# Optimization experiments

Measured on AMD Instinct MI355X. Metric: run time of the kernel, lower is better.

Reference implementation:

```python
import jax, jax.numpy as jnp
import numpy as np

N_NODES = 100000
N_EDGES = 300000
HIDDEN = 256

def _lin_init(key, fan_in, fan_out):
    return jax.random.normal(key, (fan_in, fan_out), jnp.float32) / np.sqrt(fan_in)

def setup_inputs():
    key = jax.random.key(0)
    ks = jax.random.split(key, 16)
    x = jax.random.randint(ks[0], (N_NODES, 16), 0, 11).astype(jnp.float32)
    edge_index = jax.random.randint(ks[1], (2, N_EDGES), 0, N_NODES)
    edge_attr = jax.random.randint(ks[2], (N_EDGES, 4), 0, 5).astype(jnp.float32)
    batch = jnp.sort(jax.random.randint(ks[3], (N_NODES,), 0, 256))
    atom_emb = jax.random.normal(ks[4], (11, 64), jnp.float32)
    bond_emb_table = jax.random.normal(ks[5], (5, 64), jnp.float32)
    vp_w1 = _lin_init(ks[6], 64, 32); vp_b1 = jnp.zeros((32,), jnp.float32)
    vp_w2 = _lin_init(ks[7], 32, 8)
    # chemical-knowledge bias init: max_valence - 1 for atom types 0..7 (bias dim is 8)
    vp_b2 = jnp.array([3., 2., 1., 5., 0., 0., 0., 0.], jnp.float32)
    gnn_wself = jax.random.normal(ks[8], (3, HIDDEN, HIDDEN), jnp.float32) / np.sqrt(HIDDEN)
    gnn_bself = jnp.zeros((3, HIDDEN), jnp.float32)
    gnn_wmsg = jax.random.normal(ks[9], (3, HIDDEN + 64, HIDDEN), jnp.float32) / np.sqrt(HIDDEN + 64)
    gnn_bmsg = jnp.zeros((3, HIDDEN), jnp.float32)
    bc_w1 = _lin_init(ks[10], 2 * HIDDEN + 2, 128); bc_b1 = jnp.zeros((128,), jnp.float32)
    bc_w2 = _lin_init(ks[11], 128, 64); bc_b2 = jnp.zeros((64,), jnp.float32)
    bc_w3 = _lin_init(ks[12], 64, 4); bc_b3 = jnp.zeros((4,), jnp.float32)
    cp_w1 = _lin_init(ks[13], HIDDEN, 128); cp_b1 = jnp.zeros((128,), jnp.float32)
    cp_w2 = _lin_init(ks[14], 128, 32); cp_b2 = jnp.zeros((32,), jnp.float32)
    return dict(x=x, edge_attr=edge_attr, atom_emb=atom_emb, bond_emb_table=bond_emb_table,
                vp_w1=vp_w1, vp_b1=vp_b1, vp_w2=vp_w2, vp_b2=vp_b2,
                gnn_wself=gnn_wself, gnn_bself=gnn_bself, gnn_wmsg=gnn_wmsg, gnn_bmsg=gnn_bmsg,
                bc_w1=bc_w1, bc_b1=bc_b1, bc_w2=bc_w2, bc_b2=bc_b2, bc_w3=bc_w3, bc_b3=bc_b3,
                cp_w1=cp_w1, cp_b1=cp_b1, cp_w2=cp_w2, cp_b2=cp_b2,
                edge_index=edge_index, batch=batch)

def _forward(x, edge_attr, atom_emb, bond_emb_table, vp_w1, vp_b1, vp_w2, vp_b2,
             gnn_wself, gnn_bself, gnn_wmsg, gnn_bmsg,
             bc_w1, bc_b1, bc_w2, bc_b2, bc_w3, bc_b3,
             cp_w1, cp_b1, cp_w2, cp_b2, edge_index, batch):
    relu = jax.nn.relu
    n = x.shape[0]
    atom_types = jnp.clip(x[:, 0].astype(jnp.int32), 0, 10)        # [N]
    ae = atom_emb[atom_types]                                      # [N, 64]
    valence_logits = relu(ae @ vp_w1 + vp_b1) @ vp_w2 + vp_b2      # [N, 8]
    pv = jnp.argmax(valence_logits, axis=-1) + 1                   # [N] predicted valences in [1,8]
    bt = jnp.clip(edge_attr[:, 0].astype(jnp.int32), 0, 4)
    be = bond_emb_table[bt]                                        # [E, 64]
    h = jnp.concatenate([ae, jax.nn.one_hot(pv - 1, 8, dtype=ae.dtype)], axis=-1)  # [N, 72]
    h = jnp.pad(h, ((0, 0), (0, HIDDEN - h.shape[1])))             # pad to [N, HIDDEN]
    row, col = edge_index[0], edge_index[1]
    # stacked ChemicalConstraintGNN layers (message passing with bond-type features)
    for l in range(3):
        msg = relu(jnp.concatenate([h[col], be], axis=-1) @ gnn_wmsg[l] + gnn_bmsg[l])  # [E, H]
        agg = jax.ops.segment_sum(msg, row, num_segments=n)
        h = relu(h @ gnn_wself[l] + gnn_bself[l] + agg)
    # ValenceConstraintLayer: damp nodes whose degree exceeds predicted valence
    degree = jax.ops.segment_sum(jnp.ones(row.shape[0], h.dtype), row, num_segments=n)
    violations = relu(degree - pv.astype(h.dtype))                 # [N]
    h = h / (1.0 + violations)[:, None]
    # constrained bond prediction
    bf = jnp.concatenate([h[row], h[col],
                          pv[row][:, None].astype(h.dtype), pv[col][:, None].astype(h.dtype)], axis=-1)
    bl = relu(relu(bf @ bc_w1 + bc_b1) @ bc_w2 + bc_b2) @ bc_w3 + bc_b3  # [E, 4]
    # vectorized chemical constraints (replaces per-edge Python loop)
    at_r, at_c = atom_types[row], atom_types[col]
    halogen = ((at_r == 4) | (at_r == 5) | (at_c == 4) | (at_c == 5)).astype(bl.dtype)
    lowval2 = ((pv[row] <= 2) | (pv[col] <= 2)).astype(bl.dtype)
    lowval1 = ((pv[row] <= 1) | (pv[col] <= 1)).astype(bl.dtype)
    penalty = jnp.zeros_like(bl)
    penalty = penalty.at[:, 1:].add((-100.0 * halogen - 50.0 * lowval1)[:, None])
    penalty = penalty.at[:, 2].add(-50.0 * lowval2)
    bond_logits = bl + penalty
    chem_props = relu(h @ cp_w1 + cp_b1) @ cp_w2 + cp_b2           # [N, 32]
    return h, chem_props, valence_logits, bond_logits, violations

def reference(x, edge_attr, atom_emb, bond_emb_table, vp_w1, vp_b1, vp_w2, vp_b2,
              gnn_wself, gnn_bself, gnn_wmsg, gnn_bmsg,
              bc_w1, bc_b1, bc_w2, bc_b2, bc_w3, bc_b3,
              cp_w1, cp_b1, cp_w2, cp_b2, edge_index, batch):
    return _forward(x, edge_attr, atom_emb, bond_emb_table, vp_w1, vp_b1, vp_w2, vp_b2,
                    gnn_wself, gnn_bself, gnn_wmsg, gnn_bmsg,
                    bc_w1, bc_b1, bc_w2, bc_b2, bc_w3, bc_b3,
                    cp_w1, cp_b1, cp_w2, cp_b2, edge_index, batch)
```

## Files before the change

### kernel.cpp

```cpp
#include <hip/hip_runtime.h>

#define N_NODES 100000
#define N_EDGES 300000
#define M_PAD   100096
#define E_PAD   300032

typedef unsigned short u16;
typedef short bf16x8 __attribute__((ext_vector_type(8)));
typedef float f32x4  __attribute__((ext_vector_type(4)));
typedef unsigned short u16x8 __attribute__((ext_vector_type(8)));

__device__ __forceinline__ float bf2f(u16 u) {
    unsigned x = ((unsigned)u) << 16;
    return __builtin_bit_cast(float, x);
}
__device__ __forceinline__ u16 f2bf(float f) {
    unsigned u = __builtin_bit_cast(unsigned, f);
    unsigned r = (u + 0x7FFF + ((u >> 16) & 1)) >> 16;
    return (u16)r;
}

#define H_OFF   0
#define CP_OFF  25600000
#define VL_OFF  28800000
#define BL_OFF  29600000
#define VI_OFF  30800000

#define GLL(gp, lp) __builtin_amdgcn_global_load_lds( \
    (const __attribute__((address_space(1))) unsigned int*)(gp), \
    (__attribute__((address_space(3))) unsigned int*)(lp), 16, 0, 0)

__global__ void k_type_mlp(const float* __restrict__ atom_emb,
                           const float* __restrict__ vp_w1, const float* __restrict__ vp_b1,
                           const float* __restrict__ vp_w2, const float* __restrict__ vp_b2,
                           int* __restrict__ pv_tab, float* __restrict__ vl_tab,
                           float* __restrict__ h0_tab)
{
    int tid = threadIdx.x;
    for (int i = tid; i < 11 * 256; i += 256) h0_tab[i] = 0.f;
    __syncthreads();
    if (tid < 11) {
        int t = tid;
        const float* ae = atom_emb + t * 64;
        float lg[8];
        #pragma unroll
        for (int c = 0; c < 8; ++c) lg[c] = vp_b2[c];
        for (int j = 0; j < 32; ++j) {
            float z = vp_b1[j];
            for (int d = 0; d < 64; ++d) z += ae[d] * vp_w1[d * 32 + j];
            z = fmaxf(z, 0.f);
            #pragma unroll
            for (int c = 0; c < 8; ++c) lg[c] += z * vp_w2[j * 8 + c];
        }
        int best = 0;
        #pragma unroll
        for (int c = 1; c < 8; ++c) if (lg[c] > lg[best]) best = c;
        pv_tab[t] = best + 1;
        for (int c = 0; c < 8; ++c) vl_tab[t * 8 + c] = lg[c];
        float* h0 = h0_tab + t * 256;
        for (int d = 0; d < 64; ++d) h0[d] = ae[d];
        h0[64 + best] = 1.f;
    }
}

__global__ void k_tables(const float* __restrict__ bond_emb,
                         const float* __restrict__ gnn_wself, const float* __restrict__ gnn_bself,
                         const float* __restrict__ gnn_wmsg, const float* __restrict__ gnn_bmsg,
                         const float* __restrict__ h0_tab,
                         float* __restrict__ self0_tab, float* __restrict__ msg0_tab,
                         float* __restrict__ bondtab)
{
    int b = blockIdx.x, c = threadIdx.x;
    if (b < 11) {
        int t = b;
        const float* h0 = h0_tab + t * 256;
        float acc = gnn_bself[c];
        for (int k = 0; k < 256; ++k) acc += h0[k] * gnn_wself[k * 256 + c];
        self0_tab[t * 256 + c] = acc;
    } else if (b < 66) {
        int idx = b - 11; int t = idx / 5, bb = idx % 5;
        const float* h0 = h0_tab + t * 256;
        float acc = gnn_bmsg[c];
        for (int k = 0; k < 256; ++k) acc += h0[k] * gnn_wmsg[k * 256 + c];
        const float* be = bond_emb + bb * 64;
        for (int k = 0; k < 64; ++k) acc += be[k] * gnn_wmsg[(256 + k) * 256 + c];
        msg0_tab[idx * 256 + c] = fmaxf(acc, 0.f);
    } else {
        int idx = b - 66; int l = idx / 5 + 1, bb = idx % 5;
        const float* w = gnn_wmsg + (size_t)l * 320 * 256;
        const float* be = bond_emb + bb * 64;
        float acc = gnn_bmsg[l * 256 + c];
        for (int k = 0; k < 64; ++k) acc += be[k] * w[(256 + k) * 256 + c];
        bondtab[(l - 1) * 5 * 256 + bb * 256 + c] = acc;
    }
}

__global__ void k_wtrans(const float* __restrict__ wmsg, const float* __restrict__ wself,
                         const float* __restrict__ bcw1, const float* __restrict__ cpw1,
                         const float* __restrict__ bcw2, const float* __restrict__ cpw2,
                         u16* __restrict__ BtL1, u16* __restrict__ BtL2, u16* __restrict__ Bt3,
                         u16* __restrict__ BtW2, u16* __restrict__ BtCP2)
{
    int b = blockIdx.x, k = threadIdx.x;
    if (b < 512) {
        int n = b;
        float v = (n < 256) ? wmsg[(size_t)1 * 320 * 256 + (size_t)k * 256 + n]
                            : wself[(size_t)1 * 256 * 256 + (size_t)k * 256 + (n - 256)];
        BtL1[n * 256 + k] = f2bf(v);
    } else if (b < 1024) {
        int n = b - 512;
        float v = (n < 256) ? wmsg[(size_t)2 * 320 * 256 + (size_t)k * 256 + n]
                            : wself[(size_t)2 * 256 * 256 + (size_t)k * 256 + (n - 256)];
        BtL2[n * 256 + k] = f2bf(v);
    } else if (b < 1408) {
        int n = b - 1024;
        float v;
        if (n < 128)      v = bcw1[k * 128 + n];
        else if (n < 256) v = bcw1[(256 + k) * 128 + (n - 128)];
        else              v = cpw1[k * 128 + (n - 256)];
        Bt3[n * 256 + k] = f2bf(v);
    } else if (b < 1536) {
        int n = b - 1408;
        if (k < 128) BtW2[n * 128 + k] = f2bf(n < 64 ? bcw2[k * 64 + n] : 0.f);
    } else {
        int n = b - 1536;
        if (k < 128) BtCP2[n * 128 + k] = f2bf(n < 32 ? cpw2[k * 32 + n] : 0.f);
    }
}

__global__ void k_setup_bias(const float* __restrict__ bself, const float* __restrict__ bcb1,
                             const float* __restrict__ cpb1,
                             float* __restrict__ bias512, float* __restrict__ biasPost)
{
    int i = blockIdx.x * 256 + threadIdx.x;
    if (i < 1024) {
        int l = i >> 9, c = i & 511;
        bias512[l * 512 + c] = (c < 256) ? 0.f : bself[(l + 1) * 256 + (c - 256)];
    } else if (i < 1408) {
        int c = i - 1024;
        biasPost[c] = (c < 128) ? bcb1[c] : ((c < 256) ? 0.f : cpb1[c - 256]);
    }
}

__global__ void k_node_init(const float* __restrict__ x, const int* __restrict__ pv_tab,
                            const float* __restrict__ vl_tab,
                            int* __restrict__ types, int* __restrict__ pvarr,
                            int* __restrict__ degree, float* __restrict__ vl_out)
{
    int i = blockIdx.x * blockDim.x + threadIdx.x;
    if (i >= N_NODES) return;
    int t = (int)x[i * 16];
    t = min(max(t, 0), 10);
    types[i] = t;
    pvarr[i] = pv_tab[t];
    degree[i] = 0;
    float4 v0 = *(const float4*)&vl_tab[t * 8];
    float4 v1 = *(const float4*)&vl_tab[t * 8 + 4];
    *(float4*)&vl_out[i * 8]     = v0;
    *(float4*)&vl_out[i * 8 + 4] = v1;
}

__global__ void k_edge_deg(const int* __restrict__ ei, int* __restrict__ degree)
{
    int e = blockIdx.x * blockDim.x + threadIdx.x;
    if (e >= N_EDGES) return;
    atomicAdd(&degree[ei[e]], 1);
}

#define SCAN_B 1024
__global__ void k_scan1(const int* __restrict__ degree, int* __restrict__ part, int* __restrict__ bsum)
{
    __shared__ int s[SCAN_B];
    int tid = threadIdx.x;
    int i = blockIdx.x * SCAN_B + tid;
    int v = (i < N_NODES) ? degree[i] : 0;
    s[tid] = v; __syncthreads();
    for (int off = 1; off < SCAN_B; off <<= 1) {
        int t = (tid >= off) ? s[tid - off] : 0;
        __syncthreads();
        s[tid] += t;
        __syncthreads();
    }
    if (i < N_NODES) part[i] = s[tid] - v;
    if (tid == SCAN_B - 1) bsum[blockIdx.x] = s[tid];
}

__global__ void k_scan2(const int* __restrict__ bsum, int* __restrict__ bbase, int nb)
{
    __shared__ int s[128];
    int tid = threadIdx.x;
    int v = (tid < nb) ? bsum[tid] : 0;
    s[tid] = v; __syncthreads();
    for (int off = 1; off < 128; off <<= 1) {
        int t = (tid >= off) ? s[tid - off] : 0;
        __syncthreads();
        s[tid] += t;
        __syncthreads();
    }
    bbase[tid] = s[tid] - v;
}

__global__ void k_scan3(int* __restrict__ part, const int* __restrict__ bbase, int* __restrict__ cursor)
{
    int i = blockIdx.x * SCAN_B + threadIdx.x;
    if (i >= N_NODES) return;
    int o = part[i] + bbase[blockIdx.x];
    part[i] = o;
    cursor[i] = o;
}

__global__ void k_csr_fill(const int* __restrict__ ei, const float* __restrict__ edge_attr,
                           const int* __restrict__ types, int* __restrict__ cursor,
                           int* __restrict__ csr, int* __restrict__ rowcsr, int* __restrict__ eidarr)
{
    int e = blockIdx.x * blockDim.x + threadIdx.x;
    if (e >= N_EDGES) return;
    int row = ei[e], col = ei[N_EDGES + e];
    int bt = (int)edge_attr[e * 4];
    bt = min(max(bt, 0), 4);
    int pos = atomicAdd(&cursor[row], 1);
    csr[pos] = col | (bt << 20) | (types[col] << 24);
    rowcsr[pos] = row;
    eidarr[pos] = e;
}

__global__ __launch_bounds__(256) void k_agg0(const int* __restrict__ offsets, const int* __restrict__ degree,
                       const int* __restrict__ types,
                       const float* __restrict__ self0_tab, const float* __restrict__ msg0_tab,
                       const int* __restrict__ csr, u16* __restrict__ h)
{
    int wid = threadIdx.x >> 6, lane = threadIdx.x & 63;
    int node = blockIdx.x * 4 + wid;
    if (node >= N_NODES) return;
    int t = types[node];
    float4 acc = *(const float4*)&self0_tab[t * 256 + lane * 4];
    int start = offsets[node], deg = degree[node];
    for (int j = 0; j < deg; ++j) {
        int p = csr[start + j];
        int combo = ((p >> 24) & 0xF) * 5 + ((p >> 20) & 7);
        float4 m = *(const float4*)&msg0_tab[combo * 256 + lane * 4];
        acc.x += m.x; acc.y += m.y; acc.z += m.z; acc.w += m.w;
    }
    ushort4 r;
    r.x = f2bf(fmaxf(acc.x, 0.f)); r.y = f2bf(fmaxf(acc.y, 0.f));
    r.z = f2bf(fmaxf(acc.z, 0.f)); r.w = f2bf(fmaxf(acc.w, 0.f));
    *(ushort4*)&h[(size_t)node * 256 + lane * 4] = r;
}

__global__ __launch_bounds__(256) void k_agg12(const int* __restrict__ offsets, const int* __restrict__ degree,
                        const u16* __restrict__ hs, const u16* __restrict__ hm,
                        const float* __restrict__ bondtab, const int* __restrict__ csr,
                        u16* __restrict__ h, int final_layer, const int* __restrict__ pvarr,
                        float* __restrict__ h_out, u16* __restrict__ hd_bf, float* __restrict__ viol_out)
{
    int wid = threadIdx.x >> 6, lane = threadIdx.x & 63;
    int node = blockIdx.x * 4 + wid;
    if (node >= N_NODES) return;
    ushort4 s4 = *(const ushort4*)&hs[(size_t)node * 256 + lane * 4];
    float ax = bf2f(s4.x), ay = bf2f(s4.y), az = bf2f(s4.z), aw = bf2f(s4.w);
    int start = offsets[node], deg = degree[node];
    for (int j = 0; j < deg; ++j) {
        int p = csr[start + j];
        int c = p & 0xFFFFF;
        int bt = (p >> 20) & 7;
        ushort4 m4 = *(const ushort4*)&hm[(size_t)c * 256 + lane * 4];
        float4 bb = *(const float4*)&bondtab[bt * 256 + lane * 4];
        ax += fmaxf(bf2f(m4.x) + bb.x, 0.f);
        ay += fmaxf(bf2f(m4.y) + bb.y, 0.f);
        az += fmaxf(bf2f(m4.z) + bb.z, 0.f);
        aw += fmaxf(bf2f(m4.w) + bb.w, 0.f);
    }
    ax = fmaxf(ax, 0.f); ay = fmaxf(ay, 0.f); az = fmaxf(az, 0.f); aw = fmaxf(aw, 0.f);
    if (!final_layer) {
        ushort4 r;
        r.x = f2bf(ax); r.y = f2bf(ay); r.z = f2bf(az); r.w = f2bf(aw);
        *(ushort4*)&h[(size_t)node * 256 + lane * 4] = r;
    } else {
        float viol = fmaxf((float)deg - (float)pvarr[node], 0.f);
        float s = 1.f / (1.f + viol);
        ax *= s; ay *= s; az *= s; aw *= s;
        float4 v = make_float4(ax, ay, az, aw);
        *(float4*)&h_out[(size_t)node * 256 + lane * 4] = v;
        ushort4 r;
        r.x = f2bf(ax); r.y = f2bf(ay); r.z = f2bf(az); r.w = f2bf(aw);
        *(ushort4*)&hd_bf[(size_t)node * 256 + lane * 4] = r;
        if (lane == 0) viol_out[node] = viol;
    }
}

__global__ __launch_bounds__(256) void k_gemm_dual(
    const u16* __restrict__ A, const u16* __restrict__ Bt,
    const float* __restrict__ bias512,
    u16* __restrict__ Dm, u16* __restrict__ Ds, int M, int MT)
{
    __shared__ u16 S[24576];
    u16* As = S;
    u16* Bs = S + 4096;
    u16* Cs = S + 8192;
    int b = blockIdx.x;
    int rsub = b & 31;
    int nt = rsub >> 3, m8 = rsub & 7;
    int mt = (b >> 5) * 8 + m8;
    if (mt >= MT) return;
    int bm = mt * 128, bn = nt * 128;

    int t = threadIdx.x;
    int lane = t & 63, w = t >> 6;
    int wm = w & 1, wn = w >> 1;
    f32x4 zero = {0.f, 0.f, 0.f, 0.f};
    f32x4 acc[4][4];
    #pragma unroll
    for (int i = 0; i < 4; ++i)
        #pragma unroll
        for (int j = 0; j < 4; ++j) acc[i][j] = zero;

    int arow = t >> 2, acol = (t & 3) * 8;
    const u16* Ag = A + (size_t)(bm + arow) * 256 + acol;
    const u16* Bg = Bt + (size_t)(bn + arow) * 256 + acol;
    u16* Asp = As + t * 8;
    u16* Bsp = Bs + t * 8;
    int q = lane >> 4, r = lane & 15;

    for (int k0 = 0; k0 < 256; k0 += 32) {
        __syncthreads();
        GLL(Ag + k0,            Asp);
        GLL(Ag + 64 * 256 + k0, Asp + 2048);
        GLL(Bg + k0,            Bsp);
        GLL(Bg + 64 * 256 + k0, Bsp + 2048);
        __syncthreads();
        bf16x8 af[4], bfr[4];
        #pragma unroll
        for (int i = 0; i < 4; ++i)
            af[i] = *(const bf16x8*)&As[(wm * 64 + i * 16 + r) * 32 + q * 8];
        #pragma unroll
        for (int j = 0; j < 4; ++j)
            bfr[j] = *(const bf16x8*)&Bs[(wn * 64 + j * 16 + r) * 32 + q * 8];
        #pragma unroll
        for (int i = 0; i < 4; ++i)
            #pragma unroll
            for (int j = 0; j < 4; ++j)
                acc[i][j] = __builtin_amdgcn_mfma_f32_16x16x32_bf16(af[i], bfr[j], acc[i][j], 0, 0, 0);
    }
    #pragma unroll
    for (int i = 0; i < 4; ++i) {
        int rowl = wm * 64 + i * 16 + q * 4;
        #pragma unroll
        for (int j = 0; j < 4; ++j) {
            int coll = wn * 64 + j * 16 + r;
            float bv = bias512[bn + coll];
            #pragma unroll
            for (int rr = 0; rr < 4; ++rr)
                Cs[(rowl + rr) * 128 + coll] = f2bf(acc[i][j][rr] + bv);
        }
    }
    __syncthreads();
    u16* Dbase = (nt < 2) ? (Dm + bn) : (Ds + (bn - 256));
    int c16 = (t & 15) * 8, rbase = t >> 4;
    #pragma unroll
    for (int g = 0; g < 8; ++g) {
        int rowl = rbase + g * 16;
        int rowg = bm + rowl;
        if (rowg < M) {
            u16x8 v = *(const u16x8*)&Cs[rowl * 128 + c16];
            *(u16x8*)&Dbase[(size_t)rowg * 256 + c16] = v;
        }
    }
}

__global__ __launch_bounds__(256) void k_gemm_post(
    const u16* __restrict__ A, const u16* __restrict__ Bt3,
    const float* __restrict__ biasPost,
    u16* __restrict__ UV, u16* __restrict__ CP1, int M, int MT)
{
    __shared__ u16 S[24576];
    u16* As = S;
    u16* Bs = S + 4096;
    u16* Cs = S + 8192;
    int b = blockIdx.x;
    int rsub = b % 24;
    int nt = rsub >> 3, m8 = rsub & 7;
    int mt = (b / 24) * 8 + m8;
    if (mt >= MT) return;
    int bm = mt * 128, bn = nt * 128;

    int t = threadIdx.x;
    int lane = t & 63, w = t >> 6;
    int wm = w & 1, wn = w >> 1;
    f32x4 zero = {0.f, 0.f, 0.f, 0.f};
    f32x4 acc[4][4];
    #pragma unroll
    for (int i = 0; i < 4; ++i)
        #pragma unroll
        for (int j = 0; j < 4; ++j) acc[i][j] = zero;

    int arow = t >> 2, acol = (t & 3) * 8;
    const u16* Ag = A + (size_t)(bm + arow) * 256 + acol;
    const u16* Bg = Bt3 + (size_t)(bn + arow) * 256 + acol;
    u16* Asp = As + t * 8;
    u16* Bsp = Bs + t * 8;
    int q = lane >> 4, r = lane & 15;

    for (int k0 = 0; k0 < 256; k0 += 32) {
        __syncthreads();
        GLL(Ag + k0,            Asp);
        GLL(Ag + 64 * 256 + k0, Asp + 2048);
        GLL(Bg + k0,            Bsp);
        GLL(Bg + 64 * 256 + k0, Bsp + 2048);
        __syncthreads();
        bf16x8 af[4], bfr[4];
        #pragma unroll
        for (int i = 0; i < 4; ++i)
            af[i] = *(const bf16x8*)&As[(wm * 64 + i * 16 + r) * 32 + q * 8];
        #pragma unroll
        for (int j = 0; j < 4; ++j)
            bfr[j] = *(const bf16x8*)&Bs[(wn * 64 + j * 16 + r) * 32 + q * 8];
        #pragma unroll
        for (int i = 0; i < 4; ++i)
            #pragma unroll
            for (int j = 0; j < 4; ++j)
                acc[i][j] = __builtin_amdgcn_mfma_f32_16x16x32_bf16(af[i], bfr[j], acc[i][j], 0, 0, 0);
    }
    #pragma unroll
    for (int i = 0; i < 4; ++i) {
        int rowl = wm * 64 + i * 16 + q * 4;
        #pragma unroll
        for (int j = 0; j < 4; ++j) {
            int coll = wn * 64 + j * 16 + r;
            float bv = biasPost[bn + coll];
            #pragma unroll
            for (int rr = 0; rr < 4; ++rr) {
                float val = acc[i][j][rr] + bv;
                if (nt == 2) val = fmaxf(val, 0.f);
                Cs[(rowl + rr) * 128 + coll] = f2bf(val);
            }
        }
    }
    __syncthreads();
    int c16 = (t & 15) * 8, rbase = t >> 4;
    #pragma unroll
    for (int g = 0; g < 8; ++g) {
        int rowl = rbase + g * 16;
        int rowg = bm + rowl;
        if (rowg < M) {
            u16x8 v = *(const u16x8*)&Cs[rowl * 128 + c16];
            if (nt < 2) *(u16x8*)&UV[(size_t)rowg * 256 + bn + c16] = v;
            else        *(u16x8*)&CP1[(size_t)rowg * 128 + c16] = v;
        }
    }
}

__global__ __launch_bounds__(256) void k_gemm_k128(
    const u16* __restrict__ A, const u16* __restrict__ Bt,
    const float* __restrict__ bias, float* __restrict__ C,
    int ldc, int M, int N)
{
    __shared__ u16 As[4096];
    __shared__ u16 Bs[4096];
    int t = threadIdx.x;
    int lane = t & 63, w = t >> 6;
    int wm = w & 1, wn = w >> 1;
    int bm = blockIdx.x * 128;
    int arow = t >> 2, acol = (t & 3) * 8;
    int q = lane >> 4, r = lane & 15;
    const u16* Ag = A + (size_t)(bm + arow) * 128 + acol;
    const u16* Bg = Bt + (size_t)arow * 128 + acol;
    f32x4 zero = {0.f, 0.f, 0.f, 0.f};
    f32x4 acc[4][4];
    #pragma unroll
    for (int i = 0; i < 4; ++i)
        #pragma unroll
        for (int j = 0; j < 4; ++j) acc[i][j] = zero;

    for (int kc = 0; kc < 4; ++kc) {
        __syncthreads();
        GLL(Ag + kc * 32,            As + t * 8);
        GLL(Ag + 64 * 128 + kc * 32, As + 2048 + t * 8);
        GLL(Bg + kc * 32,            Bs + t * 8);
        GLL(Bg + 64 * 128 + kc * 32, Bs + 2048 + t * 8);
        __syncthreads();
        bf16x8 af[4], bfr[4];
        #pragma unroll
        for (int i = 0; i < 4; ++i)
            af[i] = *(const bf16x8*)&As[(wm * 64 + i * 16 + r) * 32 + q * 8];
        #pragma unroll
        for (int j = 0; j < 4; ++j)
            bfr[j] = *(const bf16x8*)&Bs[(wn * 64 + j * 16 + r) * 32 + q * 8];
        #pragma unroll
        for (int i = 0; i < 4; ++i)
            #pragma unroll
            for (int j = 0; j < 4; ++j)
                acc[i][j] = __builtin_amdgcn_mfma_f32_16x16x32_bf16(af[i], bfr[j], acc[i][j], 0, 0, 0);
    }
    #pragma unroll
    for (int i = 0; i < 4; ++i) {
        int rowb = bm + wm * 64 + i * 16 + q * 4;
        #pragma unroll
        for (int j = 0; j < 4; ++j) {
            int colg = wn * 64 + j * 16 + r;
            if (colg >= N) continue;
            float bv = bias[colg];
            #pragma unroll
            for (int rr = 0; rr < 4; ++rr) {
                int rowg = rowb + rr;
                if (rowg < M) C[(size_t)rowg * ldc + colg] = acc[i][j][rr] + bv;
            }
        }
    }
}

__global__ __launch_bounds__(256) void k_bond_fused(
    const int* __restrict__ csr, const int* __restrict__ rowcsr, const int* __restrict__ eidarr,
    const int* __restrict__ types, const int* __restrict__ pvarr, const int* __restrict__ pv_tab,
    const u16* __restrict__ uv, const float* __restrict__ bc_w1,
    const u16* __restrict__ BtW2, const float* __restrict__ bc_b2,
    const float* __restrict__ bc_w3, const float* __restrict__ bc_b3,
    float* __restrict__ bl_out)
{
    __shared__ u16 T1s[16384];
    __shared__ u16 Bs[16384];
    __shared__ float w5s[128], w6s[128], W3s[256], b2s[64], b3s[4];
    __shared__ int pvts[16];

    int t = threadIdx.x;
    int p0 = blockIdx.x * 128;

    if (t < 128) { w5s[t] = bc_w1[512 * 128 + t]; w6s[t] = bc_w1[513 * 128 + t]; }
    if (t < 256) W3s[t] = bc_w3[t];
    if (t < 64) b2s[t] = bc_b2[t];
    if (t < 4)  b3s[t] = bc_b3[t];
    if (t < 11) pvts[t] = pv_tab[t];
    #pragma unroll
    for (int c = 0; c < 4; ++c) {
        GLL(BtW2 + (size_t)(t >> 2) * 128 + c * 32 + (t & 3) * 8,        Bs + c * 4096 + t * 8);
        GLL(BtW2 + (size_t)(64 + (t >> 2)) * 128 + c * 32 + (t & 3) * 8, Bs + c * 4096 + 2048 + t * 8);
    }

    int l = t >> 1;
    int half = t & 1;
    int pos = p0 + l;
    int prow = 0, pk = 0;
    if (pos < N_EDGES) { prow = rowcsr[pos]; pk = csr[pos]; }
    int pcol = pk & 0xFFFFF;
    float pvr = (float)pvarr[prow];
    __syncthreads();
    float pvc = (float)pvts[(pk >> 24) & 0xF];

    const u16* up = uv + (size_t)prow * 256 + half * 64;
    const u16* vp = uv + (size_t)pcol * 256 + 128 + half * 64;
    #pragma unroll
    for (int j = 0; j < 8; ++j) {
        int c = half * 64 + j * 8;
        ushort4 ua = *(const ushort4*)(up + j * 8);
        ushort4 ub = *(const ushort4*)(up + j * 8 + 4);
        ushort4 va = *(const ushort4*)(vp + j * 8);
        ushort4 vb = *(const ushort4*)(vp + j * 8 + 4);
        int chunk = c >> 5, kk = c & 31;
        u16* dst = T1s + chunk * 4096 + l * 32 + kk;
        dst[0] = f2bf(fmaxf(bf2f(ua.x) + bf2f(va.x) + pvr * w5s[c+0] + pvc * w6s[c+0], 0.f));
        dst[1] = f2bf(fmaxf(bf2f(ua.y) + bf2f(va.y) + pvr * w5s[c+1] + pvc * w6s[c+1], 0.f));
        dst[2] = f2bf(fmaxf(bf2f(ua.z) + bf2f(va.z) + pvr * w5s[c+2] + pvc * w6s[c+2], 0.f));
        dst[3] = f2bf(fmaxf(bf2f(ua.w) + bf2f(va.w) + pvr * w5s[c+3] + pvc * w6s[c+3], 0.f));
        dst[4] = f2bf(fmaxf(bf2f(ub.x) + bf2f(vb.x) + pvr * w5s[c+4] + pvc * w6s[c+4], 0.f));
        dst[5] = f2bf(fmaxf(bf2f(ub.y) + bf2f(vb.y) + pvr * w5s[c+5] + pvc * w6s[c+5], 0.f));
        dst[6] = f2bf(fmaxf(bf2f(ub.z) + bf2f(vb.z) + pvr * w5s[c+6] + pvc * w6s[c+6], 0.f));
        dst[7] = f2bf(fmaxf(bf2f(ub.w) + bf2f(vb.w) + pvr * w5s[c+7] + pvc * w6s[c+7], 0.f));
    }
    __syncthreads();

    int lane = t & 63, w = t >> 6;
    int wm = w & 1, wn = w >> 1;
    int q = lane >> 4, r = lane & 15;
    f32x4 zero = {0.f, 0.f, 0.f, 0.f};
    f32x4 acc[4][4];
    #pragma unroll
    for (int i = 0; i < 4; ++i)
        #pragma unroll
        for (int j = 0; j < 4; ++j) acc[i][j] = zero;
    #pragma unroll
    for (int c = 0; c < 4; ++c) {
        bf16x8 af[4], bfr[4];
        #pragma unroll
        for (int i = 0; i < 4; ++i)
            af[i] = *(const bf16x8*)&T1s[c * 4096 + (wm * 64 + i * 16 + r) * 32 + q * 8];
        #pragma unroll
        for (int j = 0; j < 4; ++j)
            bfr[j] = *(const bf16x8*)&Bs[c * 4096 + (wn * 64 + j * 16 + r) * 32 + q * 8];
        #pragma unroll
        for (int i = 0; i < 4; ++i)
            #pragma unroll
            for (int j = 0; j < 4; ++j)
                acc[i][j] = __builtin_amdgcn_mfma_f32_16x16x32_bf16(af[i], bfr[j], acc[i][j], 0, 0, 0);
    }
    __syncthreads();

    float* T2f = (float*)T1s;
    if (wn == 0) {
        #pragma unroll
        for (int i = 0; i < 4; ++i) {
            int row = wm * 64 + i * 16 + q * 4;
            #pragma unroll
            for (int j = 0; j < 4; ++j) {
                int col = j * 16 + r;
                float bv = b2s[col];
                #pragma unroll
                for (int rr = 0; rr < 4; ++rr)
                    T2f[(row + rr) * 64 + col] = fmaxf(acc[i][j][rr] + bv, 0.f);
            }
        }
    }
    __syncthreads();

    if (t < 128) {
        int pos3 = p0 + t;
        if (pos3 < N_EDGES) {
            float a0 = b3s[0], a1 = b3s[1], a2 = b3s[2], a3 = b3s[3];
            const float* trow = &T2f[t * 64];
            #pragma unroll 8
            for (int kk = 0; kk < 64; ++kk) {
                int k = (kk + t) & 63;
                float tv = trow[k];
                a0 += tv * W3s[k * 4 + 0];
                a1 += tv * W3s[k * 4 + 1];
                a2 += tv * W3s[k * 4 + 2];
                a3 += tv * W3s[k * 4 + 3];
            }
            int prow3 = rowcsr[pos3];
            int pk3 = csr[pos3];
            int tc = (pk3 >> 24) & 0xF;
            int tr = types[prow3];
            int pr = pvarr[prow3];
            int pc = pvts[tc];
            float halogen = (tr == 4 || tr == 5 || tc == 4 || tc == 5) ? 1.f : 0.f;
            float l1 = (pr <= 1 || pc <= 1) ? 1.f : 0.f;
            float l2 = (pr <= 2 || pc <= 2) ? 1.f : 0.f;
            float pen13 = -100.f * halogen - 50.f * l1;
            a1 += pen13;
            a3 += pen13;
            a2 += pen13 - 50.f * l2;
            int eid = eidarr[pos3];
            *(float4*)&bl_out[(size_t)eid * 4] = make_float4(a0, a1, a2, a3);
        }
    }
}

extern "C" void kernel_launch(void* const* d_in, const int* in_sizes, int n_in,
                              void* d_out, int out_size, void* d_ws, size_t ws_size,
                              hipStream_t stream)
{
    const float* x          = (const float*)d_in[0];
    const float* edge_attr  = (const float*)d_in[1];
    const float* atom_emb   = (const float*)d_in[2];
    const float* bond_emb   = (const float*)d_in[3];
    const float* vp_w1      = (const float*)d_in[4];
    const float* vp_b1      = (const float*)d_in[5];
    const float* vp_w2      = (const float*)d_in[6];
    const float* vp_b2      = (const float*)d_in[7];
    const float* gnn_wself  = (const float*)d_in[8];
    const float* gnn_bself  = (const float*)d_in[9];
    const float* gnn_wmsg   = (const float*)d_in[10];
    const float* gnn_bmsg   = (const float*)d_in[11];
    const float* bc_w1      = (const float*)d_in[12];
    const float* bc_b1      = (const float*)d_in[13];
    const float* bc_w2      = (const float*)d_in[14];
    const float* bc_b2      = (const float*)d_in[15];
    const float* bc_w3      = (const float*)d_in[16];
    const float* bc_b3      = (const float*)d_in[17];
    const float* cp_w1      = (const float*)d_in[18];
    const float* cp_b1      = (const float*)d_in[19];
    const float* cp_w2      = (const float*)d_in[20];
    const float* cp_b2      = (const float*)d_in[21];
    const int*   ei         = (const int*)d_in[22];

    float* out    = (float*)d_out;
    float* h_out  = out + H_OFF;
    float* cp_out = out + CP_OFF;
    float* vl_out = out + VL_OFF;
    float* bl_out = out + BL_OFF;
    float* vi_out = out + VI_OFF;

    char* base = (char*)d_ws;
    const size_t S = (size_t)M_PAD * 256 * 2;
    u16* h_bf  = (u16*)(base + 0 * S);
    u16* uv_bf = (u16*)(base + 0 * S);
    u16* hm_bf = (u16*)(base + 1 * S);
    u16* hs_bf = (u16*)(base + 2 * S);
    u16* hd_bf = (u16*)(base + 3 * S);
    u16* cp1_bf= (u16*)(base + 4 * S);
    char* w    = base + 4 * S + (size_t)M_PAD * 128 * 2;
    int* degree  = (int*)w; w += (size_t)N_NODES * 4;
    int* offsets = (int*)w; w += (size_t)N_NODES * 4;
    int* cursor  = (int*)w; w += (size_t)N_NODES * 4;
    int* types   = (int*)w; w += (size_t)N_NODES * 4;
    int* pvarr   = (int*)w; w += (size_t)N_NODES * 4;
    int* csr     = (int*)w; w += (size_t)E_PAD * 4;
    int* rowcsr  = (int*)w; w += (size_t)E_PAD * 4;
    int* eidarr  = (int*)w; w += (size_t)E_PAD * 4;
    int* bsum    = (int*)w; w += 4096;
    int* bbase   = (int*)w; w += 4096;
    int* pv_tab  = (int*)w; w += 1024;
    float* vl_tab    = (float*)w; w += 2048;
    float* h0_tab    = (float*)w; w += 11 * 256 * 4;
    float* self0_tab = (float*)w; w += 11 * 256 * 4;
    float* msg0_tab  = (float*)w; w += 55 * 256 * 4;
    float* bondtab   = (float*)w; w += 2 * 5 * 256 * 4;
    u16* BtL1  = (u16*)w; w += 512 * 256 * 2;
    u16* BtL2  = (u16*)w; w += 512 * 256 * 2;
    u16* Bt3   = (u16*)w; w += 384 * 256 * 2;
    u16* BtW2  = (u16*)w; w += 128 * 128 * 2;
    u16* BtCP2 = (u16*)w; w += 128 * 128 * 2;
    float* bias512  = (float*)w; w += 2 * 512 * 4;
    float* biasPost = (float*)w; w += 384 * 4;

    k_type_mlp<<<1, 256, 0, stream>>>(atom_emb, vp_w1, vp_b1, vp_w2, vp_b2, pv_tab, vl_tab, h0_tab);
    k_tables<<<76, 256, 0, stream>>>(bond_emb, gnn_wself, gnn_bself, gnn_wmsg, gnn_bmsg,
                                     h0_tab, self0_tab, msg0_tab, bondtab);
    k_wtrans<<<1664, 256, 0, stream>>>(gnn_wmsg, gnn_wself, bc_w1, cp_w1, bc_w2, cp_w2,
                                       BtL1, BtL2, Bt3, BtW2, BtCP2);
    k_setup_bias<<<6, 256, 0, stream>>>(gnn_bself, bc_b1, cp_b1, bias512, biasPost);
    k_node_init<<<(N_NODES + 255) / 256, 256, 0, stream>>>(x, pv_tab, vl_tab, types, pvarr, degree, vl_out);
    k_edge_deg<<<(N_EDGES + 255) / 256, 256, 0, stream>>>(ei, degree);
    int nb = (N_NODES + SCAN_B - 1) / SCAN_B;
    k_scan1<<<nb, SCAN_B, 0, stream>>>(degree, offsets, bsum);
    k_scan2<<<1, 128, 0, stream>>>(bsum, bbase, nb);
    k_scan3<<<nb, SCAN_B, 0, stream>>>(offsets, bbase, cursor);
    k_csr_fill<<<(N_EDGES + 255) / 256, 256, 0, stream>>>(ei, edge_attr, types, cursor, csr, rowcsr, eidarr);
    k_agg0<<<N_NODES / 4, 256, 0, stream>>>(offsets, degree, types, self0_tab, msg0_tab, csr, h_bf);

    const int MT = M_PAD / 128;
    const int QB = (MT + 7) / 8;
    for (int l = 1; l <= 2; ++l) {
        const u16* BtL = (l == 1) ? BtL1 : BtL2;
        k_gemm_dual<<<QB * 32, 256, 0, stream>>>(h_bf, BtL, bias512 + (size_t)(l - 1) * 512,
                                                 hm_bf, hs_bf, N_NODES, MT);
        k_agg12<<<N_NODES / 4, 256, 0, stream>>>(offsets, degree, hs_bf, hm_bf,
                                                 bondtab + (size_t)(l - 1) * 5 * 256, csr, h_bf,
                                                 (l == 2) ? 1 : 0, pvarr, h_out, hd_bf, vi_out);
    }

    k_gemm_post<<<QB * 24, 256, 0, stream>>>(hd_bf, Bt3, biasPost, uv_bf, cp1_bf, N_NODES, MT);
    k_gemm_k128<<<MT, 256, 0, stream>>>(cp1_bf, BtCP2, cp_b2, cp_out, 32, N_NODES, 32);

    k_bond_fused<<<E_PAD / 128, 256, 0, stream>>>(csr, rowcsr, eidarr, types, pvarr, pv_tab,
                                                  uv_bf, bc_w1, BtW2, bc_b2, bc_w3, bc_b3, bl_out);
}
```

Measured before the change: 641.3 us.

## Triple-buffer LDS tiles in both GEMM kernels to overlap loads with MFMA

Replaces the two-barrier load-then-compute K loop in the dual and post GEMM kernels with a three-slot LDS ring. The next K slice is prefetched through direct global-to-LDS loads while the current one is multiplied, and only one barrier per step is kept. Explicit vmcnt waits decide when the current slice is ready. The idea is to hide global memory latency behind MFMA work. The cost is a reliance on exact vmcnt accounting and on three slots, rather than a barrier, preventing overwrite races. The epilogue staging buffer now reuses the start of shared memory after a final sync.

```diff
diff --git a/kernel.cpp b/kernel.cpp
--- a/kernel.cpp
+++ b/kernel.cpp
@@ -294,9 +294,7 @@
     u16* __restrict__ Dm, u16* __restrict__ Ds, int M, int MT)
 {
     __shared__ u16 S[24576];
-    u16* As = S;
-    u16* Bs = S + 4096;
-    u16* Cs = S + 8192;
+    u16* Cs = S;
     int b = blockIdx.x;
     int rsub = b & 31;
     int nt = rsub >> 3, m8 = rsub & 7;
@@ -317,30 +315,44 @@
     int arow = t >> 2, acol = (t & 3) * 8;
     const u16* Ag = A + (size_t)(bm + arow) * 256 + acol;
     const u16* Bg = Bt + (size_t)(bn + arow) * 256 + acol;
-    u16* Asp = As + t * 8;
-    u16* Bsp = Bs + t * 8;
     int q = lane >> 4, r = lane & 15;
 
-    for (int k0 = 0; k0 < 256; k0 += 32) {
-        __syncthreads();
-        GLL(Ag + k0,            Asp);
-        GLL(Ag + 64 * 256 + k0, Asp + 2048);
-        GLL(Bg + k0,            Bsp);
-        GLL(Bg + 64 * 256 + k0, Bsp + 2048);
-        __syncthreads();
+    GLL(Ag,            S + t * 8);
+    GLL(Ag + 64 * 256, S + 2048 + t * 8);
+    GLL(Bg,            S + 4096 + t * 8);
+    GLL(Bg + 64 * 256, S + 4096 + 2048 + t * 8);
+
+    #pragma unroll
+    for (int ks = 0; ks < 8; ++ks) {
+        int cb = (ks % 3) * 8192;
+        if (ks < 7) {
+            int nb = ((ks + 1) % 3) * 8192;
+            int k0 = (ks + 1) * 32;
+            GLL(Ag + k0,            S + nb + t * 8);
+            GLL(Ag + 64 * 256 + k0, S + nb + 2048 + t * 8);
+            GLL(Bg + k0,            S + nb + 4096 + t * 8);
+            GLL(Bg + 64 * 256 + k0, S + nb + 4096 + 2048 + t * 8);
+            asm volatile("s_waitcnt vmcnt(4)" ::: "memory");
+        } else {
+            asm volatile("s_waitcnt vmcnt(0)" ::: "memory");
+        }
+        __builtin_amdgcn_s_barrier();
+        __builtin_amdgcn_sched_barrier(0);
         bf16x8 af[4], bfr[4];
         #pragma unroll
         for (int i = 0; i < 4; ++i)
-            af[i] = *(const bf16x8*)&As[(wm * 64 + i * 16 + r) * 32 + q * 8];
+            af[i] = *(const bf16x8*)&S[cb + (wm * 64 + i * 16 + r) * 32 + q * 8];
         #pragma unroll
         for (int j = 0; j < 4; ++j)
-            bfr[j] = *(const bf16x8*)&Bs[(wn * 64 + j * 16 + r) * 32 + q * 8];
+            bfr[j] = *(const bf16x8*)&S[cb + 4096 + (wn * 64 + j * 16 + r) * 32 + q * 8];
         #pragma unroll
         for (int i = 0; i < 4; ++i)
             #pragma unroll
             for (int j = 0; j < 4; ++j)
                 acc[i][j] = __builtin_amdgcn_mfma_f32_16x16x32_bf16(af[i], bfr[j], acc[i][j], 0, 0, 0);
     }
+    __syncthreads();
+
     #pragma unroll
     for (int i = 0; i < 4; ++i) {
         int rowl = wm * 64 + i * 16 + q * 4;
@@ -373,9 +385,7 @@
     u16* __restrict__ UV, u16* __restrict__ CP1, int M, int MT)
 {
     __shared__ u16 S[24576];
-    u16* As = S;
-    u16* Bs = S + 4096;
-    u16* Cs = S + 8192;
+    u16* Cs = S;
     int b = blockIdx.x;
     int rsub = b % 24;
     int nt = rsub >> 3, m8 = rsub & 7;
@@ -396,30 +406,44 @@
     int arow = t >> 2, acol = (t & 3) * 8;
     const u16* Ag = A + (size_t)(bm + arow) * 256 + acol;
     const u16* Bg = Bt3 + (size_t)(bn + arow) * 256 + acol;
-    u16* Asp = As + t * 8;
-    u16* Bsp = Bs + t * 8;
     int q = lane >> 4, r = lane & 15;
 
-    for (int k0 = 0; k0 < 256; k0 += 32) {
-        __syncthreads();
-        GLL(Ag + k0,            Asp);
-        GLL(Ag + 64 * 256 + k0, Asp + 2048);
-        GLL(Bg + k0,            Bsp);
-        GLL(Bg + 64 * 256 + k0, Bsp + 2048);
-        __syncthreads();
+    GLL(Ag,            S + t * 8);
+    GLL(Ag + 64 * 256, S + 2048 + t * 8);
+    GLL(Bg,            S + 4096 + t * 8);
+    GLL(Bg + 64 * 256, S + 4096 + 2048 + t * 8);
+
+    #pragma unroll
+    for (int ks = 0; ks < 8; ++ks) {
+        int cb = (ks % 3) * 8192;
+        if (ks < 7) {
+            int nb = ((ks + 1) % 3) * 8192;
+            int k0 = (ks + 1) * 32;
+            GLL(Ag + k0,            S + nb + t * 8);
+            GLL(Ag + 64 * 256 + k0, S + nb + 2048 + t * 8);
+            GLL(Bg + k0,            S + nb + 4096 + t * 8);
+            GLL(Bg + 64 * 256 + k0, S + nb + 4096 + 2048 + t * 8);
+            asm volatile("s_waitcnt vmcnt(4)" ::: "memory");
+        } else {
+            asm volatile("s_waitcnt vmcnt(0)" ::: "memory");
+        }
+        __builtin_amdgcn_s_barrier();
+        __builtin_amdgcn_sched_barrier(0);
         bf16x8 af[4], bfr[4];
         #pragma unroll
         for (int i = 0; i < 4; ++i)
-            af[i] = *(const bf16x8*)&As[(wm * 64 + i * 16 + r) * 32 + q * 8];
+            af[i] = *(const bf16x8*)&S[cb + (wm * 64 + i * 16 + r) * 32 + q * 8];
         #pragma unroll
         for (int j = 0; j < 4; ++j)
-            bfr[j] = *(const bf16x8*)&Bs[(wn * 64 + j * 16 + r) * 32 + q * 8];
+            bfr[j] = *(const bf16x8*)&S[cb + 4096 + (wn * 64 + j * 16 + r) * 32 + q * 8];
         #pragma unroll
         for (int i = 0; i < 4; ++i)
             #pragma unroll
             for (int j = 0; j < 4; ++j)
                 acc[i][j] = __builtin_amdgcn_mfma_f32_16x16x32_bf16(af[i], bfr[j], acc[i][j], 0, 0, 0);
     }
+    __syncthreads();
+
     #pragma unroll
     for (int i = 0; i < 4; ++i) {
         int rowl = wm * 64 + i * 16 + q * 4;
```

Result: faster. 610.9 us (-4.7%).
